# Kernel tuning notes

Measured on AMD Instinct MI355X. Metric: run time of the kernel, lower is better.

## Reference

```python
import jax, jax.numpy as jnp
import numpy as np


def _lstm_dir(xz, Uh, reverse):
    """Run one LSTM direction. xz: [B,T,4U] = x@W + b precomputed. Uh: [U,4U].
    activation='sigmoid' (replaces tanh on candidate and cell output),
    recurrent_activation='sigmoid' (Keras default). Gate order: i, f, g, o."""
    B = xz.shape[0]
    units = Uh.shape[0]
    h0 = jnp.zeros((B, units), xz.dtype)
    c0 = jnp.zeros((B, units), xz.dtype)

    def step(carry, z_t):
        h, c = carry
        z = z_t + h @ Uh                      # [B,4U]
        i, f, g, o = jnp.split(z, 4, axis=-1)
        i = jax.nn.sigmoid(i)
        f = jax.nn.sigmoid(f)
        g = jax.nn.sigmoid(g)                 # activation='sigmoid'
        o = jax.nn.sigmoid(o)
        c = f * c + i * g
        h = o * jax.nn.sigmoid(c)             # output activation also sigmoid
        return (h, c), h

    xz_t = jnp.swapaxes(xz, 0, 1)             # [T,B,4U]
    _, hs = jax.lax.scan(step, (h0, c0), xz_t, reverse=reverse)
    return jnp.swapaxes(hs, 0, 1)             # [B,T,U], time-ordered


def setup_inputs() -> dict:
    key = jax.random.key(0)
    k1, k2, k3 = jax.random.split(key, 3)
    B, T, D = 16, 1024, 1024
    L, U = 5, 512
    x = jax.random.normal(k1, (B, T, D), dtype=jnp.float32)
    # Glorot-ish scaling to keep sigmoids out of deep saturation
    W = jax.random.normal(k2, (L, 2, D, 4 * U), dtype=jnp.float32) * 0.03
    Uh = jax.random.normal(k3, (L, 2, U, 4 * U), dtype=jnp.float32) * 0.03
    b = jnp.zeros((L, 2, 4 * U), dtype=jnp.float32)
    return {"x": x, "W": W, "Uh": Uh, "b": b}


def reference(x, W, Uh, b):
    y = x
    n_layers = W.shape[0]
    for l in range(n_layers):
        outs = []
        for d, rev in ((0, False), (1, True)):
            # input projection for all timesteps at once (one big GEMM)
            xz = jnp.einsum('bti,io->bto', y, W[l, d]) + b[l, d]
            outs.append(_lstm_dir(xz, Uh[l, d], rev))
        y = jnp.concatenate(outs, axis=-1)    # Bidirectional merge_mode='concat'
    return y
```

## Files before the change

kernel.cpp:

```cpp
#include <hip/hip_runtime.h>
#include <hip/hip_bf16.h>
#include <stdint.h>


typedef __attribute__((ext_vector_type(8))) short short8;
typedef __attribute__((ext_vector_type(4))) float f32x4;

union U128 { uint4 u; short8 s; };
static __device__ __forceinline__ short8 as_short8(uint4 v) { U128 x; x.u = v; return x.s; }

static __device__ __forceinline__ float sigf(float x) { return 1.0f / (1.0f + __expf(-x)); }

static __device__ __forceinline__ uint32_t f2bfbits(float f) {
  union { float f; uint32_t u; } x; x.f = f;
  return (x.u + 0x7fffu + ((x.u >> 16) & 1u)) >> 16;
}
static __device__ __forceinline__ float bflo(uint32_t v) {
  union { uint32_t u; float f; } x; x.u = v << 16; return x.f;
}
static __device__ __forceinline__ float bfhi(uint32_t v) {
  union { uint32_t u; float f; } x; x.u = v & 0xffff0000u; return x.f;
}

__global__ __launch_bounds__(256) void f32_to_bf16_k(const float* __restrict__ in,
                                                     __hip_bfloat16* __restrict__ out,
                                                     int n4) {
  int i = blockIdx.x * 256 + threadIdx.x;
  if (i < n4) {
    float4 v = ((const float4*)in)[i];
    uint32_t lo = f2bfbits(v.x) | (f2bfbits(v.y) << 16);
    uint32_t hi = f2bfbits(v.z) | (f2bfbits(v.w) << 16);
    ((uint2*)out)[i] = make_uint2(lo, hi);
  }
}

__global__ __launch_bounds__(256) void transpose_bf16_k(const float* __restrict__ in,
                                                        __hip_bfloat16* __restrict__ outp,
                                                        int R) {
  __shared__ float tile[64][65];
  int d = blockIdx.z;
  int k0 = blockIdx.x * 64;
  int c0 = blockIdx.y * 64;
  const float* inb = in + (size_t)d * R * 2048;
  __hip_bfloat16* ob = outp + (size_t)d * 2048 * R;
  int col = threadIdx.x & 63, rr = threadIdx.x >> 6;
#pragma unroll
  for (int i = 0; i < 16; ++i) {
    int r = rr + i * 4;
    tile[r][col] = inb[(size_t)(k0 + r) * 2048 + c0 + col];
  }
  __syncthreads();
#pragma unroll
  for (int i = 0; i < 16; ++i) {
    int r = rr + i * 4;
    ob[(size_t)(c0 + r) * R + k0 + col] = __float2bfloat16(tile[col][r]);
  }
}

__global__ __launch_bounds__(256) void gemm_xz_k(const __hip_bfloat16* __restrict__ y,
                                                 const __hip_bfloat16* __restrict__ Wt,
                                                 const float* __restrict__ bias,
                                                 __hip_bfloat16* __restrict__ xz) {
  __shared__ uint4 Asl[8 * 2 * 64];
  __shared__ uint4 Bsl[8 * 2 * 64];
  int m0 = blockIdx.x * 128;
  int dir = blockIdx.y >> 4;
  int n0 = (blockIdx.y & 15) * 128;
  int tid = threadIdx.x, lane = tid & 63, wv = tid >> 6;
  int wm = wv & 1, wn = wv >> 1;
  const __hip_bfloat16* Wd = Wt + (size_t)dir * 2048 * 1024;
  f32x4 acc[4][4] = {};
  for (int kb = 0; kb < 1024; kb += 64) {
    __syncthreads();
#pragma unroll
    for (int i = 0; i < 4; ++i) {
      int slot = i * 256 + tid;
      int ln = slot & 63, kc = (slot >> 6) & 1, mt = slot >> 7;
      int row = mt * 16 + (ln & 15);
      int kk = kc * 32 + (ln >> 4) * 8;
      Asl[slot] = *(const uint4*)(y + (size_t)(m0 + row) * 1024 + kb + kk);
      Bsl[slot] = *(const uint4*)(Wd + (size_t)(n0 + row) * 1024 + kb + kk);
    }
    __syncthreads();
#pragma unroll
    for (int kc = 0; kc < 2; ++kc) {
      short8 af[4], bf[4];
#pragma unroll
      for (int i = 0; i < 4; ++i) {
        af[i] = as_short8(Asl[((wm * 4 + i) * 2 + kc) * 64 + lane]);
        bf[i] = as_short8(Bsl[((wn * 4 + i) * 2 + kc) * 64 + lane]);
      }
#pragma unroll
      for (int i = 0; i < 4; ++i)
#pragma unroll
        for (int j = 0; j < 4; ++j)
          acc[i][j] = __builtin_amdgcn_mfma_f32_16x16x32_bf16(af[i], bf[j], acc[i][j], 0, 0, 0);
    }
  }
  int cq = lane >> 4, cn = lane & 15;
#pragma unroll
  for (int i = 0; i < 4; ++i)
#pragma unroll
    for (int j = 0; j < 4; ++j) {
      int n_g = n0 + (wn * 4 + j) * 16 + cn;
      int q = n_g >> 9, u = n_g & 511, swg = u >> 5, jj = u & 31;
      float bv = bias[dir * 2048 + n_g];
#pragma unroll
      for (int r = 0; r < 4; ++r) {
        int m = m0 + (wm * 4 + i) * 16 + cq * 4 + r;
        int b = m >> 10, t = m & 1023;
        size_t addr = (((size_t)(dir * 16 + swg) * 1024 + t) * 2048) + (q * 16 + b) * 32 + jj;
        xz[addr] = __float2bfloat16(acc[i][j][r] + bv);
      }
    }
}

__global__ __launch_bounds__(256) void lstm_rec_k(const __hip_bfloat16* __restrict__ Ut,
                                                  const __hip_bfloat16* __restrict__ xz,
                                                  __hip_bfloat16* __restrict__ ynext,
                                                  float* __restrict__ outf) {
  extern __shared__ char smem[];
  uint4* uh = (uint4*)smem;
  __hip_bfloat16* hbuf = (__hip_bfloat16*)(smem + 131072);
  float* zbuf = (float*)(smem + 147712);
  __hip_bfloat16* xbuf = (__hip_bfloat16*)(smem + 155904);
  int dir = blockIdx.x & 1;
  int swg = blockIdx.x >> 1;
  int u0 = swg * 32;
  int tid = threadIdx.x, lane = tid & 63, wv = tid >> 6;
  int quad = lane >> 4, l15 = lane & 15;
  const __hip_bfloat16* Ud = Ut + (size_t)dir * 2048 * 512;

#pragma unroll 4
  for (int i = 0; i < 32; ++i) {
    int slot = i * 256 + tid;
    int ls = slot & 63, kc = (slot >> 6) & 15, nt = slot >> 10;
    int n_g = (nt >> 1) * 512 + u0 + (nt & 1) * 16 + (ls & 15);
    int k = kc * 32 + (ls >> 4) * 8;
    uh[slot] = *(const uint4*)(Ud + (size_t)n_g * 512 + k);
  }
  __syncthreads();

  int nt0 = wv * 2, nt1 = wv * 2 + 1;
  int pb = tid >> 4, pj = (tid & 15) * 2;
  float c0 = 0.f, c1 = 0.f;

  int t0 = dir ? 1023 : 0;
  const uint4* xp0 = (const uint4*)(xz + ((size_t)(dir * 16 + swg) * 1024 + t0) * 2048) + tid;
  uint4 xcur = *xp0;

  for (int s = 0; s < 1024; ++s) {
    int t = dir ? (1023 - s) : s;
    uint4 xnxt;
    if (s < 1023) {
      int tn = dir ? (1022 - s) : (s + 1);
      xnxt = *((const uint4*)(xz + ((size_t)(dir * 16 + swg) * 1024 + tn) * 2048) + tid);
    }
    f32x4 z0 = {}, z1 = {};
    if (s > 0) {
      int tprev = dir ? (t + 1) : (t - 1);
      unsigned long long hv[8];
      const unsigned long long* gp[8];
#pragma unroll
      for (int i = 0; i < 4; ++i) {
        int v = i * 2048 + tid * 8;
        int b = v >> 9, col = v & 511;
        const unsigned long long* g =
            (const unsigned long long*)(ynext + ((size_t)b * 1024 + tprev) * 1024 + dir * 512 + col);
        gp[2 * i] = g;
        gp[2 * i + 1] = g + 1;
      }
#pragma unroll
      for (int i = 0; i < 8; ++i)
        hv[i] = __hip_atomic_load(gp[i], __ATOMIC_RELAXED, __HIP_MEMORY_SCOPE_AGENT);
      for (;;) {
        bool ok = true;
#pragma unroll
        for (int i = 0; i < 8; ++i)
          ok &= ((uint32_t)hv[i] != 0u) && ((uint32_t)(hv[i] >> 32) != 0u);
        if (ok) break;
#pragma unroll
        for (int i = 0; i < 8; ++i)
          if (((uint32_t)hv[i] == 0u) || ((uint32_t)(hv[i] >> 32) == 0u))
            hv[i] = __hip_atomic_load(gp[i], __ATOMIC_RELAXED, __HIP_MEMORY_SCOPE_AGENT);
      }
#pragma unroll
      for (int i = 0; i < 4; ++i) {
        int v = i * 2048 + tid * 8;
        int b = v >> 9, col = v & 511;
        unsigned long long* lp = (unsigned long long*)(hbuf + b * 520 + col);
        lp[0] = hv[2 * i];
        lp[1] = hv[2 * i + 1];
      }
      __syncthreads();
#pragma unroll
      for (int kc = 0; kc < 16; ++kc) {
        short8 afrag = *(const short8*)(hbuf + l15 * 520 + kc * 32 + quad * 8);
        z0 = __builtin_amdgcn_mfma_f32_16x16x32_bf16(afrag, as_short8(uh[(nt0 * 16 + kc) * 64 + lane]), z0, 0, 0, 0);
        z1 = __builtin_amdgcn_mfma_f32_16x16x32_bf16(afrag, as_short8(uh[(nt1 * 16 + kc) * 64 + lane]), z1, 0, 0, 0);
      }
    }
#pragma unroll
    for (int r = 0; r < 4; ++r) {
      int m = quad * 4 + r;
      zbuf[m * 128 + nt0 * 16 + l15] = z0[r];
      zbuf[m * 128 + nt1 * 16 + l15] = z1[r];
    }
    *(uint4*)(xbuf + tid * 8) = xcur;
    __syncthreads();
    const float* zb = zbuf + pb * 128;
    uint32_t xi = *(const uint32_t*)(xbuf + (0 * 16 + pb) * 32 + pj);
    uint32_t xf = *(const uint32_t*)(xbuf + (1 * 16 + pb) * 32 + pj);
    uint32_t xg = *(const uint32_t*)(xbuf + (2 * 16 + pb) * 32 + pj);
    uint32_t xo = *(const uint32_t*)(xbuf + (3 * 16 + pb) * 32 + pj);
    float i0 = sigf(zb[pj] + bflo(xi)),      i1 = sigf(zb[pj + 1] + bfhi(xi));
    float f0 = sigf(zb[32 + pj] + bflo(xf)), f1 = sigf(zb[32 + pj + 1] + bfhi(xf));
    float g0 = sigf(zb[64 + pj] + bflo(xg)), g1 = sigf(zb[64 + pj + 1] + bfhi(xg));
    float o0 = sigf(zb[96 + pj] + bflo(xo)), o1 = sigf(zb[96 + pj + 1] + bfhi(xo));
    c0 = f0 * c0 + i0 * g0;
    c1 = f1 * c1 + i1 * g1;
    float h0 = o0 * sigf(c0);
    float h1 = o1 * sigf(c1);
    size_t oidx = ((size_t)pb * 1024 + t) * 1024 + dir * 512 + u0 + pj;
    uint32_t ha = f2bfbits(h0); ha += (ha == 0u);
    uint32_t hb = f2bfbits(h1); hb += (hb == 0u);
    uint32_t hp = ha | (hb << 16);
    __hip_atomic_store((uint32_t*)(ynext + oidx), hp, __ATOMIC_RELAXED, __HIP_MEMORY_SCOPE_AGENT);
    if (outf) { outf[oidx] = h0; outf[oidx + 1] = h1; }
    __syncthreads();
    xcur = xnxt;
  }
}

extern "C" void kernel_launch(void* const* d_in, const int* in_sizes, int n_in,
                              void* d_out, int out_size, void* d_ws, size_t ws_size,
                              hipStream_t stream) {
  const float* x  = (const float*)d_in[0];
  const float* W  = (const float*)d_in[1];
  const float* Uh = (const float*)d_in[2];
  const float* b  = (const float*)d_in[3];

  char* ws = (char*)d_ws;
  size_t off = 0;
  __hip_bfloat16* yA = (__hip_bfloat16*)(ws + off); off += (size_t)16 * 1024 * 1024 * 2;
  __hip_bfloat16* yB = (__hip_bfloat16*)(ws + off); off += (size_t)16 * 1024 * 1024 * 2;
  __hip_bfloat16* xz = (__hip_bfloat16*)(ws + off); off += (size_t)2 * 16 * 1024 * 2048 * 2;
  __hip_bfloat16* Wt = (__hip_bfloat16*)(ws + off); off += (size_t)2 * 2048 * 1024 * 2;
  __hip_bfloat16* Ut = (__hip_bfloat16*)(ws + off); off += (size_t)2 * 2048 * 512 * 2;

  f32_to_bf16_k<<<dim3(16384), dim3(256), 0, stream>>>(x, yA, 4194304);
  hipFuncSetAttribute(reinterpret_cast<const void*>(lstm_rec_k),
                      hipFuncAttributeMaxDynamicSharedMemorySize, 160000);
  for (int l = 0; l < 5; ++l) {
    transpose_bf16_k<<<dim3(16, 32, 2), dim3(256), 0, stream>>>(W + (size_t)l * 2 * 1024 * 2048, Wt, 1024);
    transpose_bf16_k<<<dim3(8, 32, 2),  dim3(256), 0, stream>>>(Uh + (size_t)l * 2 * 512 * 2048, Ut, 512);
    __hip_bfloat16* ycur = (l & 1) ? yB : yA;
    __hip_bfloat16* ynxt = (l & 1) ? yA : yB;
    hipMemsetAsync(ynxt, 0, (size_t)16 * 1024 * 1024 * 2, stream);
    gemm_xz_k<<<dim3(128, 32), dim3(256), 0, stream>>>(ycur, Wt, b + (size_t)l * 2 * 2048, xz);
    lstm_rec_k<<<dim3(32), dim3(256), 160000, stream>>>(
        Ut, xz, ynxt, (l == 4) ? (float*)d_out : nullptr);
  }
}
```

Baseline: 13.86 ms.

## Load recurrent h fragments straight into MFMA registers, dropping LDS staging and barriers

Each lane now polls the exact 16 bytes of the previous hidden state it needs as the MFMA A-operand, straight from global memory. This removes the LDS h-buffer, one __syncthreads, and the end-of-step barrier, which becomes a compiler-only fence. It relies on the cross-block spin-wait to order reuse of zbuf and xbuf across steps. The zbuf row stride is padded to 132 to reduce bank conflicts. The trade-off is more redundant global and L2 loads per step, since all four waves fetch the same fragment, and more registers held during polling.

```diff
diff --git a/kernel.cpp b/kernel.cpp
--- a/kernel.cpp
+++ b/kernel.cpp
@@ -9,6 +9,8 @@
 union U128 { uint4 u; short8 s; };
 static __device__ __forceinline__ short8 as_short8(uint4 v) { U128 x; x.u = v; return x.s; }
 
+union U128Q { unsigned long long q[2]; short8 s; };
+
 static __device__ __forceinline__ float sigf(float x) { return 1.0f / (1.0f + __expf(-x)); }
 
 static __device__ __forceinline__ uint32_t f2bfbits(float f) {
@@ -20,6 +22,10 @@
 }
 static __device__ __forceinline__ float bfhi(uint32_t v) {
   union { uint32_t u; float f; } x; x.u = v & 0xffff0000u; return x.f;
+}
+
+static __device__ __forceinline__ bool qok(unsigned long long v) {
+  return ((uint32_t)v != 0u) & ((uint32_t)(v >> 32) != 0u);
 }
 
 __global__ __launch_bounds__(256) void f32_to_bf16_k(const float* __restrict__ in,
@@ -121,9 +127,8 @@
                                                   float* __restrict__ outf) {
   extern __shared__ char smem[];
   uint4* uh = (uint4*)smem;
-  __hip_bfloat16* hbuf = (__hip_bfloat16*)(smem + 131072);
-  float* zbuf = (float*)(smem + 147712);
-  __hip_bfloat16* xbuf = (__hip_bfloat16*)(smem + 155904);
+  float* zbuf = (float*)(smem + 131072);
+  __hip_bfloat16* xbuf = (__hip_bfloat16*)(smem + 139520);
   int dir = blockIdx.x & 1;
   int swg = blockIdx.x >> 1;
   int u0 = swg * 32;
@@ -149,6 +154,8 @@
   const uint4* xp0 = (const uint4*)(xz + ((size_t)(dir * 16 + swg) * 1024 + t0) * 2048) + tid;
   uint4 xcur = *xp0;
 
+  const char* fragbase0 = (const char*)(ynext + (size_t)l15 * 1024 * 1024 + (size_t)dir * 512 + quad * 8);
+
   for (int s = 0; s < 1024; ++s) {
     int t = dir ? (1023 - s) : s;
     uint4 xnxt;
@@ -159,56 +166,46 @@
     f32x4 z0 = {}, z1 = {};
     if (s > 0) {
       int tprev = dir ? (t + 1) : (t - 1);
-      unsigned long long hv[8];
-      const unsigned long long* gp[8];
-#pragma unroll
-      for (int i = 0; i < 4; ++i) {
-        int v = i * 2048 + tid * 8;
-        int b = v >> 9, col = v & 511;
-        const unsigned long long* g =
-            (const unsigned long long*)(ynext + ((size_t)b * 1024 + tprev) * 1024 + dir * 512 + col);
-        gp[2 * i] = g;
-        gp[2 * i + 1] = g + 1;
-      }
-#pragma unroll
-      for (int i = 0; i < 8; ++i)
-        hv[i] = __hip_atomic_load(gp[i], __ATOMIC_RELAXED, __HIP_MEMORY_SCOPE_AGENT);
+      const char* fb = fragbase0 + (size_t)tprev * 2048;
+      unsigned long long hq0[16], hq1[16];
+#pragma unroll
+      for (int kc = 0; kc < 16; ++kc) {
+        hq0[kc] = __hip_atomic_load((const unsigned long long*)(fb + kc * 64),
+                                    __ATOMIC_RELAXED, __HIP_MEMORY_SCOPE_AGENT);
+        hq1[kc] = __hip_atomic_load((const unsigned long long*)(fb + kc * 64 + 8),
+                                    __ATOMIC_RELAXED, __HIP_MEMORY_SCOPE_AGENT);
+      }
       for (;;) {
         bool ok = true;
 #pragma unroll
-        for (int i = 0; i < 8; ++i)
-          ok &= ((uint32_t)hv[i] != 0u) && ((uint32_t)(hv[i] >> 32) != 0u);
+        for (int kc = 0; kc < 16; ++kc) ok &= qok(hq0[kc]) & qok(hq1[kc]);
         if (ok) break;
 #pragma unroll
-        for (int i = 0; i < 8; ++i)
-          if (((uint32_t)hv[i] == 0u) || ((uint32_t)(hv[i] >> 32) == 0u))
-            hv[i] = __hip_atomic_load(gp[i], __ATOMIC_RELAXED, __HIP_MEMORY_SCOPE_AGENT);
-      }
-#pragma unroll
-      for (int i = 0; i < 4; ++i) {
-        int v = i * 2048 + tid * 8;
-        int b = v >> 9, col = v & 511;
-        unsigned long long* lp = (unsigned long long*)(hbuf + b * 520 + col);
-        lp[0] = hv[2 * i];
-        lp[1] = hv[2 * i + 1];
-      }
-      __syncthreads();
+        for (int kc = 0; kc < 16; ++kc) {
+          if (!qok(hq0[kc]))
+            hq0[kc] = __hip_atomic_load((const unsigned long long*)(fb + kc * 64),
+                                        __ATOMIC_RELAXED, __HIP_MEMORY_SCOPE_AGENT);
+          if (!qok(hq1[kc]))
+            hq1[kc] = __hip_atomic_load((const unsigned long long*)(fb + kc * 64 + 8),
+                                        __ATOMIC_RELAXED, __HIP_MEMORY_SCOPE_AGENT);
+        }
+      }
 #pragma unroll
       for (int kc = 0; kc < 16; ++kc) {
-        short8 afrag = *(const short8*)(hbuf + l15 * 520 + kc * 32 + quad * 8);
-        z0 = __builtin_amdgcn_mfma_f32_16x16x32_bf16(afrag, as_short8(uh[(nt0 * 16 + kc) * 64 + lane]), z0, 0, 0, 0);
-        z1 = __builtin_amdgcn_mfma_f32_16x16x32_bf16(afrag, as_short8(uh[(nt1 * 16 + kc) * 64 + lane]), z1, 0, 0, 0);
+        U128Q a; a.q[0] = hq0[kc]; a.q[1] = hq1[kc];
+        z0 = __builtin_amdgcn_mfma_f32_16x16x32_bf16(a.s, as_short8(uh[(nt0 * 16 + kc) * 64 + lane]), z0, 0, 0, 0);
+        z1 = __builtin_amdgcn_mfma_f32_16x16x32_bf16(a.s, as_short8(uh[(nt1 * 16 + kc) * 64 + lane]), z1, 0, 0, 0);
       }
     }
 #pragma unroll
     for (int r = 0; r < 4; ++r) {
       int m = quad * 4 + r;
-      zbuf[m * 128 + nt0 * 16 + l15] = z0[r];
-      zbuf[m * 128 + nt1 * 16 + l15] = z1[r];
+      zbuf[m * 132 + nt0 * 16 + l15] = z0[r];
+      zbuf[m * 132 + nt1 * 16 + l15] = z1[r];
     }
     *(uint4*)(xbuf + tid * 8) = xcur;
     __syncthreads();
-    const float* zb = zbuf + pb * 128;
+    const float* zb = zbuf + pb * 132;
     uint32_t xi = *(const uint32_t*)(xbuf + (0 * 16 + pb) * 32 + pj);
     uint32_t xf = *(const uint32_t*)(xbuf + (1 * 16 + pb) * 32 + pj);
     uint32_t xg = *(const uint32_t*)(xbuf + (2 * 16 + pb) * 32 + pj);
@@ -227,7 +224,7 @@
     uint32_t hp = ha | (hb << 16);
     __hip_atomic_store((uint32_t*)(ynext + oidx), hp, __ATOMIC_RELAXED, __HIP_MEMORY_SCOPE_AGENT);
     if (outf) { outf[oidx] = h0; outf[oidx + 1] = h1; }
-    __syncthreads();
+    asm volatile("" ::: "memory");
     xcur = xnxt;
   }
 }
@@ -250,7 +247,7 @@
 
   f32_to_bf16_k<<<dim3(16384), dim3(256), 0, stream>>>(x, yA, 4194304);
   hipFuncSetAttribute(reinterpret_cast<const void*>(lstm_rec_k),
-                      hipFuncAttributeMaxDynamicSharedMemorySize, 160000);
+                      hipFuncAttributeMaxDynamicSharedMemorySize, 143616);
   for (int l = 0; l < 5; ++l) {
     transpose_bf16_k<<<dim3(16, 32, 2), dim3(256), 0, stream>>>(W + (size_t)l * 2 * 1024 * 2048, Wt, 1024);
     transpose_bf16_k<<<dim3(8, 32, 2),  dim3(256), 0, stream>>>(Uh + (size_t)l * 2 * 512 * 2048, Ut, 512);
@@ -258,7 +255,7 @@
     __hip_bfloat16* ynxt = (l & 1) ? yA : yB;
     hipMemsetAsync(ynxt, 0, (size_t)16 * 1024 * 1024 * 2, stream);
     gemm_xz_k<<<dim3(128, 32), dim3(256), 0, stream>>>(ycur, Wt, b + (size_t)l * 2 * 2048, xz);
-    lstm_rec_k<<<dim3(32), dim3(256), 160000, stream>>>(
+    lstm_rec_k<<<dim3(32), dim3(256), 143616, stream>>>(
         Ut, xz, ynxt, (l == 4) ? (float*)d_out : nullptr);
   }
 }
```

New measurement: 36.06 ms. 160% more time.

## Interleave gate columns so LSTM cell update runs in MFMA registers via shuffles

Applied to the files above, without the earlier changes.

Reorders the recurrent weight columns and the precomputed xz layout so the four gates of each unit land in adjacent lanes of the MFMA output. The cell update is then done directly from accumulator registers with lane shuffles, which removes the LDS round trip through zbuf/xbuf and one __syncthreads per timestep on the serial recurrence. It also pads the h buffer stride to change LDS bank mapping. The cost is more shuffles, redundant sigmoid work across lanes, and narrower strided stores of h.

```diff
diff --git a/kernel.cpp b/kernel.cpp
--- a/kernel.cpp
+++ b/kernel.cpp
@@ -103,13 +103,16 @@
 #pragma unroll
     for (int j = 0; j < 4; ++j) {
       int n_g = n0 + (wn * 4 + j) * 16 + cn;
-      int q = n_g >> 9, u = n_g & 511, swg = u >> 5, jj = u & 31;
+      int gate = n_g >> 9, u = n_g & 511, swg = u >> 5, ul = u & 31;
+      int nt = ul >> 2, l15 = ((ul & 3) << 2) | gate;
       float bv = bias[dir * 2048 + n_g];
 #pragma unroll
       for (int r = 0; r < 4; ++r) {
         int m = m0 + (wm * 4 + i) * 16 + cq * 4 + r;
         int b = m >> 10, t = m & 1023;
-        size_t addr = (((size_t)(dir * 16 + swg) * 1024 + t) * 2048) + (q * 16 + b) * 32 + jj;
+        int quad = b >> 2, rr = b & 3;
+        size_t addr = (((size_t)(dir * 16 + swg) * 1024 + t) * 2048) +
+                      ((nt * 16 + l15) * 4 + quad) * 4 + rr;
         xz[addr] = __float2bfloat16(acc[i][j][r] + bv);
       }
     }
@@ -122,8 +125,6 @@
   extern __shared__ char smem[];
   uint4* uh = (uint4*)smem;
   __hip_bfloat16* hbuf = (__hip_bfloat16*)(smem + 131072);
-  float* zbuf = (float*)(smem + 147712);
-  __hip_bfloat16* xbuf = (__hip_bfloat16*)(smem + 155904);
   int dir = blockIdx.x & 1;
   int swg = blockIdx.x >> 1;
   int u0 = swg * 32;
@@ -135,26 +136,35 @@
   for (int i = 0; i < 32; ++i) {
     int slot = i * 256 + tid;
     int ls = slot & 63, kc = (slot >> 6) & 15, nt = slot >> 10;
-    int n_g = (nt >> 1) * 512 + u0 + (nt & 1) * 16 + (ls & 15);
+    int n_g = (ls & 3) * 512 + u0 + nt * 4 + ((ls & 15) >> 2);
     int k = kc * 32 + (ls >> 4) * 8;
     uh[slot] = *(const uint4*)(Ud + (size_t)n_g * 512 + k);
   }
   __syncthreads();
 
   int nt0 = wv * 2, nt1 = wv * 2 + 1;
-  int pb = tid >> 4, pj = (tid & 15) * 2;
-  float c0 = 0.f, c1 = 0.f;
+  int o0 = ((nt0 * 16 + l15) * 4 + quad) * 4;
+  int o1 = ((nt1 * 16 + l15) * 4 + quad) * 4;
+  bool gb0 = (lane & 1) != 0, gb1 = (lane & 2) != 0;
+  int u4 = l15 >> 2;
+  int unit = u0 + wv * 8 + 0 ;
+  bool st_act = ((l15 & 7) == 0);
+  float cst0[4] = {0.f, 0.f, 0.f, 0.f};
+  float cst1[4] = {0.f, 0.f, 0.f, 0.f};
 
   int t0 = dir ? 1023 : 0;
-  const uint4* xp0 = (const uint4*)(xz + ((size_t)(dir * 16 + swg) * 1024 + t0) * 2048) + tid;
-  uint4 xcur = *xp0;
+  const __hip_bfloat16* xc0 = xz + ((size_t)(dir * 16 + swg) * 1024 + t0) * 2048;
+  uint2 xq0 = *(const uint2*)(xc0 + o0);
+  uint2 xq1 = *(const uint2*)(xc0 + o1);
 
   for (int s = 0; s < 1024; ++s) {
     int t = dir ? (1023 - s) : s;
-    uint4 xnxt;
+    uint2 xn0 = xq0, xn1 = xq1;
     if (s < 1023) {
       int tn = dir ? (1022 - s) : (s + 1);
-      xnxt = *((const uint4*)(xz + ((size_t)(dir * 16 + swg) * 1024 + tn) * 2048) + tid);
+      const __hip_bfloat16* xc = xz + ((size_t)(dir * 16 + swg) * 1024 + tn) * 2048;
+      xn0 = *(const uint2*)(xc + o0);
+      xn1 = *(const uint2*)(xc + o1);
     }
     f32x4 z0 = {}, z1 = {};
     if (s > 0) {
@@ -188,48 +198,57 @@
       for (int i = 0; i < 4; ++i) {
         int v = i * 2048 + tid * 8;
         int b = v >> 9, col = v & 511;
-        unsigned long long* lp = (unsigned long long*)(hbuf + b * 520 + col);
+        unsigned long long* lp = (unsigned long long*)(hbuf + b * 528 + col);
         lp[0] = hv[2 * i];
         lp[1] = hv[2 * i + 1];
       }
       __syncthreads();
 #pragma unroll
       for (int kc = 0; kc < 16; ++kc) {
-        short8 afrag = *(const short8*)(hbuf + l15 * 520 + kc * 32 + quad * 8);
+        short8 afrag = *(const short8*)(hbuf + l15 * 528 + kc * 32 + quad * 8);
         z0 = __builtin_amdgcn_mfma_f32_16x16x32_bf16(afrag, as_short8(uh[(nt0 * 16 + kc) * 64 + lane]), z0, 0, 0, 0);
         z1 = __builtin_amdgcn_mfma_f32_16x16x32_bf16(afrag, as_short8(uh[(nt1 * 16 + kc) * 64 + lane]), z1, 0, 0, 0);
       }
     }
-#pragma unroll
-    for (int r = 0; r < 4; ++r) {
-      int m = quad * 4 + r;
-      zbuf[m * 128 + nt0 * 16 + l15] = z0[r];
-      zbuf[m * 128 + nt1 * 16 + l15] = z1[r];
-    }
-    *(uint4*)(xbuf + tid * 8) = xcur;
+    float xr0[4] = {bflo(xq0.x), bfhi(xq0.x), bflo(xq0.y), bfhi(xq0.y)};
+    float xr1[4] = {bflo(xq1.x), bfhi(xq1.x), bflo(xq1.y), bfhi(xq1.y)};
+#pragma unroll
+    for (int tl = 0; tl < 2; ++tl) {
+      int unit_e = u0 + wv * 8 + (tl ? nt1 & 1 ? 0 : 0 : 0);
+#pragma unroll
+      for (int r = 0; r < 4; ++r) {
+        float zz = tl ? z1[r] : z0[r];
+        float xx = tl ? xr1[r] : xr0[r];
+        float sv = sigf(zz + xx);
+        float b1 = __shfl_xor(sv, 1);
+        float b2 = __shfl_xor(sv, 2);
+        float b3 = __shfl_xor(b1, 2);
+        float ig = gb0 ? (b1 * b3) : (sv * b2);
+        float fg = gb0 ? (gb1 ? b2 : sv) : (gb1 ? b3 : b1);
+        float og = gb0 ? (gb1 ? sv : b2) : (gb1 ? b1 : b3);
+        float& c = tl ? cst1[r] : cst0[r];
+        c = fg * c + ig;
+        float h = og * sigf(c);
+        uint32_t hb = f2bfbits(h);
+        hb += (hb == 0u);
+        uint32_t hpart = __shfl_xor(hb, 4);
+        uint32_t hfull = __float_as_uint(h);
+        uint32_t hfpart = __shfl_xor(hfull, 4);
+        if (st_act) {
+          int un = u0 + wv * 8 + (tl ? 4 : 0) + u4;
+          int batch = quad * 4 + r;
+          size_t oidx = ((size_t)batch * 1024 + t) * 1024 + dir * 512 + un;
+          __hip_atomic_store((uint32_t*)(ynext + oidx), hb | (hpart << 16),
+                             __ATOMIC_RELAXED, __HIP_MEMORY_SCOPE_AGENT);
+          if (outf) *(uint2*)(outf + oidx) = make_uint2(hfull, hfpart);
+        }
+      }
+    }
     __syncthreads();
-    const float* zb = zbuf + pb * 128;
-    uint32_t xi = *(const uint32_t*)(xbuf + (0 * 16 + pb) * 32 + pj);
-    uint32_t xf = *(const uint32_t*)(xbuf + (1 * 16 + pb) * 32 + pj);
-    uint32_t xg = *(const uint32_t*)(xbuf + (2 * 16 + pb) * 32 + pj);
-    uint32_t xo = *(const uint32_t*)(xbuf + (3 * 16 + pb) * 32 + pj);
-    float i0 = sigf(zb[pj] + bflo(xi)),      i1 = sigf(zb[pj + 1] + bfhi(xi));
-    float f0 = sigf(zb[32 + pj] + bflo(xf)), f1 = sigf(zb[32 + pj + 1] + bfhi(xf));
-    float g0 = sigf(zb[64 + pj] + bflo(xg)), g1 = sigf(zb[64 + pj + 1] + bfhi(xg));
-    float o0 = sigf(zb[96 + pj] + bflo(xo)), o1 = sigf(zb[96 + pj + 1] + bfhi(xo));
-    c0 = f0 * c0 + i0 * g0;
-    c1 = f1 * c1 + i1 * g1;
-    float h0 = o0 * sigf(c0);
-    float h1 = o1 * sigf(c1);
-    size_t oidx = ((size_t)pb * 1024 + t) * 1024 + dir * 512 + u0 + pj;
-    uint32_t ha = f2bfbits(h0); ha += (ha == 0u);
-    uint32_t hb = f2bfbits(h1); hb += (hb == 0u);
-    uint32_t hp = ha | (hb << 16);
-    __hip_atomic_store((uint32_t*)(ynext + oidx), hp, __ATOMIC_RELAXED, __HIP_MEMORY_SCOPE_AGENT);
-    if (outf) { outf[oidx] = h0; outf[oidx + 1] = h1; }
-    __syncthreads();
-    xcur = xnxt;
-  }
+    xq0 = xn0;
+    xq1 = xn1;
+  }
+  (void)unit;
 }
 
 extern "C" void kernel_launch(void* const* d_in, const int* in_sizes, int n_in,
@@ -250,7 +269,7 @@
 
   f32_to_bf16_k<<<dim3(16384), dim3(256), 0, stream>>>(x, yA, 4194304);
   hipFuncSetAttribute(reinterpret_cast<const void*>(lstm_rec_k),
-                      hipFuncAttributeMaxDynamicSharedMemorySize, 160000);
+                      hipFuncAttributeMaxDynamicSharedMemorySize, 147968);
   for (int l = 0; l < 5; ++l) {
     transpose_bf16_k<<<dim3(16, 32, 2), dim3(256), 0, stream>>>(W + (size_t)l * 2 * 1024 * 2048, Wt, 1024);
     transpose_bf16_k<<<dim3(8, 32, 2),  dim3(256), 0, stream>>>(Uh + (size_t)l * 2 * 512 * 2048, Ut, 512);
@@ -258,7 +277,7 @@
     __hip_bfloat16* ynxt = (l & 1) ? yA : yB;
     hipMemsetAsync(ynxt, 0, (size_t)16 * 1024 * 1024 * 2, stream);
     gemm_xz_k<<<dim3(128, 32), dim3(256), 0, stream>>>(ycur, Wt, b + (size_t)l * 2 * 2048, xz);
-    lstm_rec_k<<<dim3(32), dim3(256), 160000, stream>>>(
+    lstm_rec_k<<<dim3(32), dim3(256), 147968, stream>>>(
         Ut, xz, ynxt, (l == 4) ? (float*)d_out : nullptr);
   }
 }
```

Measured after the change: 21.42 ms. +54.5%, slower.

## Overlap next layer's input-projection GEMM with current LSTM recurrence in one kernel

Applied to the files above, without the earlier changes.

The recurrence kernel now launches 128 blocks. The first 32 run the sequential LSTM scan, and the other 96 compute the next layer's x@W+b GEMM tiles as soon as the needed timesteps of the current layer's output have been published. They detect readiness by polling for nonzero bf16 values with sleep-backoff spin loops. Double-buffered xz, Wt and Ut workspaces let the weight transposes and the memset move out of the critical path. The aim is to hide each layer's input-projection GEMM behind the latency-bound recurrence, which only occupies 32 CUs, at the cost of more workspace and spin-wait traffic that could contend with the recurrent blocks.

```diff
diff --git a/kernel.cpp b/kernel.cpp
--- a/kernel.cpp
+++ b/kernel.cpp
@@ -20,6 +20,9 @@
 }
 static __device__ __forceinline__ float bfhi(uint32_t v) {
   union { uint32_t u; float f; } x; x.u = v & 0xffff0000u; return x.f;
+}
+static __device__ __forceinline__ bool qok(unsigned long long v) {
+  return ((uint32_t)v != 0u) & ((uint32_t)(v >> 32) != 0u);
 }
 
 __global__ __launch_bounds__(256) void f32_to_bf16_k(const float* __restrict__ in,
@@ -108,8 +111,8 @@
 #pragma unroll
       for (int r = 0; r < 4; ++r) {
         int m = m0 + (wm * 4 + i) * 16 + cq * 4 + r;
-        int b = m >> 10, t = m & 1023;
-        size_t addr = (((size_t)(dir * 16 + swg) * 1024 + t) * 2048) + (q * 16 + b) * 32 + jj;
+        int bb = m >> 10, t = m & 1023;
+        size_t addr = (((size_t)(dir * 16 + swg) * 1024 + t) * 2048) + (q * 16 + bb) * 32 + jj;
         xz[addr] = __float2bfloat16(acc[i][j][r] + bv);
       }
     }
@@ -118,117 +121,200 @@
 __global__ __launch_bounds__(256) void lstm_rec_k(const __hip_bfloat16* __restrict__ Ut,
                                                   const __hip_bfloat16* __restrict__ xz,
                                                   __hip_bfloat16* __restrict__ ynext,
-                                                  float* __restrict__ outf) {
+                                                  float* __restrict__ outf,
+                                                  const __hip_bfloat16* __restrict__ Wtn,
+                                                  const float* __restrict__ biasn,
+                                                  __hip_bfloat16* __restrict__ xznext) {
   extern __shared__ char smem[];
-  uint4* uh = (uint4*)smem;
-  __hip_bfloat16* hbuf = (__hip_bfloat16*)(smem + 131072);
-  float* zbuf = (float*)(smem + 147712);
-  __hip_bfloat16* xbuf = (__hip_bfloat16*)(smem + 155904);
-  int dir = blockIdx.x & 1;
-  int swg = blockIdx.x >> 1;
-  int u0 = swg * 32;
   int tid = threadIdx.x, lane = tid & 63, wv = tid >> 6;
-  int quad = lane >> 4, l15 = lane & 15;
-  const __hip_bfloat16* Ud = Ut + (size_t)dir * 2048 * 512;
+
+  if (blockIdx.x < 32) {
+    uint4* uh = (uint4*)smem;
+    __hip_bfloat16* hbuf = (__hip_bfloat16*)(smem + 131072);
+    float* zbuf = (float*)(smem + 147712);
+    __hip_bfloat16* xbuf = (__hip_bfloat16*)(smem + 155904);
+    int dir = blockIdx.x & 1;
+    int swg = blockIdx.x >> 1;
+    int u0 = swg * 32;
+    int quad = lane >> 4, l15 = lane & 15;
+    const __hip_bfloat16* Ud = Ut + (size_t)dir * 2048 * 512;
 
 #pragma unroll 4
-  for (int i = 0; i < 32; ++i) {
-    int slot = i * 256 + tid;
-    int ls = slot & 63, kc = (slot >> 6) & 15, nt = slot >> 10;
-    int n_g = (nt >> 1) * 512 + u0 + (nt & 1) * 16 + (ls & 15);
-    int k = kc * 32 + (ls >> 4) * 8;
-    uh[slot] = *(const uint4*)(Ud + (size_t)n_g * 512 + k);
-  }
-  __syncthreads();
-
-  int nt0 = wv * 2, nt1 = wv * 2 + 1;
-  int pb = tid >> 4, pj = (tid & 15) * 2;
-  float c0 = 0.f, c1 = 0.f;
-
-  int t0 = dir ? 1023 : 0;
-  const uint4* xp0 = (const uint4*)(xz + ((size_t)(dir * 16 + swg) * 1024 + t0) * 2048) + tid;
-  uint4 xcur = *xp0;
-
-  for (int s = 0; s < 1024; ++s) {
-    int t = dir ? (1023 - s) : s;
-    uint4 xnxt;
-    if (s < 1023) {
-      int tn = dir ? (1022 - s) : (s + 1);
-      xnxt = *((const uint4*)(xz + ((size_t)(dir * 16 + swg) * 1024 + tn) * 2048) + tid);
-    }
-    f32x4 z0 = {}, z1 = {};
-    if (s > 0) {
-      int tprev = dir ? (t + 1) : (t - 1);
-      unsigned long long hv[8];
-      const unsigned long long* gp[8];
+    for (int i = 0; i < 32; ++i) {
+      int slot = i * 256 + tid;
+      int ls = slot & 63, kc = (slot >> 6) & 15, nt = slot >> 10;
+      int n_g = (nt >> 1) * 512 + u0 + (nt & 1) * 16 + (ls & 15);
+      int k = kc * 32 + (ls >> 4) * 8;
+      uh[slot] = *(const uint4*)(Ud + (size_t)n_g * 512 + k);
+    }
+    __syncthreads();
+
+    int nt0 = wv * 2, nt1 = wv * 2 + 1;
+    int pb = tid >> 4, pj = (tid & 15) * 2;
+    float c0 = 0.f, c1 = 0.f;
+
+    int t0 = dir ? 1023 : 0;
+    const uint4* xp0 = (const uint4*)(xz + ((size_t)(dir * 16 + swg) * 1024 + t0) * 2048) + tid;
+    uint4 xcur = *xp0;
+
+    for (int s = 0; s < 1024; ++s) {
+      int t = dir ? (1023 - s) : s;
+      uint4 xnxt;
+      if (s < 1023) {
+        int tn = dir ? (1022 - s) : (s + 1);
+        xnxt = *((const uint4*)(xz + ((size_t)(dir * 16 + swg) * 1024 + tn) * 2048) + tid);
+      }
+      f32x4 z0 = {}, z1 = {};
+      if (s > 0) {
+        int tprev = dir ? (t + 1) : (t - 1);
+        unsigned long long hv[8];
+        const unsigned long long* gp[8];
+#pragma unroll
+        for (int i = 0; i < 4; ++i) {
+          int v = i * 2048 + tid * 8;
+          int bb = v >> 9, col = v & 511;
+          const unsigned long long* g =
+              (const unsigned long long*)(ynext + ((size_t)bb * 1024 + tprev) * 1024 + dir * 512 + col);
+          gp[2 * i] = g;
+          gp[2 * i + 1] = g + 1;
+        }
+#pragma unroll
+        for (int i = 0; i < 8; ++i)
+          hv[i] = __hip_atomic_load(gp[i], __ATOMIC_RELAXED, __HIP_MEMORY_SCOPE_AGENT);
+        for (;;) {
+          bool ok = true;
+#pragma unroll
+          for (int i = 0; i < 8; ++i)
+            ok &= ((uint32_t)hv[i] != 0u) && ((uint32_t)(hv[i] >> 32) != 0u);
+          if (ok) break;
+#pragma unroll
+          for (int i = 0; i < 8; ++i)
+            if (((uint32_t)hv[i] == 0u) || ((uint32_t)(hv[i] >> 32) == 0u))
+              hv[i] = __hip_atomic_load(gp[i], __ATOMIC_RELAXED, __HIP_MEMORY_SCOPE_AGENT);
+        }
+#pragma unroll
+        for (int i = 0; i < 4; ++i) {
+          int v = i * 2048 + tid * 8;
+          int bb = v >> 9, col = v & 511;
+          unsigned long long* lp = (unsigned long long*)(hbuf + bb * 520 + col);
+          lp[0] = hv[2 * i];
+          lp[1] = hv[2 * i + 1];
+        }
+        __syncthreads();
+#pragma unroll
+        for (int kc = 0; kc < 16; ++kc) {
+          short8 afrag = *(const short8*)(hbuf + l15 * 520 + kc * 32 + quad * 8);
+          z0 = __builtin_amdgcn_mfma_f32_16x16x32_bf16(afrag, as_short8(uh[(nt0 * 16 + kc) * 64 + lane]), z0, 0, 0, 0);
+          z1 = __builtin_amdgcn_mfma_f32_16x16x32_bf16(afrag, as_short8(uh[(nt1 * 16 + kc) * 64 + lane]), z1, 0, 0, 0);
+        }
+      }
+#pragma unroll
+      for (int r = 0; r < 4; ++r) {
+        int m = quad * 4 + r;
+        zbuf[m * 128 + nt0 * 16 + l15] = z0[r];
+        zbuf[m * 128 + nt1 * 16 + l15] = z1[r];
+      }
+      *(uint4*)(xbuf + tid * 8) = xcur;
+      __syncthreads();
+      const float* zb = zbuf + pb * 128;
+      uint32_t xi = *(const uint32_t*)(xbuf + (0 * 16 + pb) * 32 + pj);
+      uint32_t xf = *(const uint32_t*)(xbuf + (1 * 16 + pb) * 32 + pj);
+      uint32_t xg = *(const uint32_t*)(xbuf + (2 * 16 + pb) * 32 + pj);
+      uint32_t xo = *(const uint32_t*)(xbuf + (3 * 16 + pb) * 32 + pj);
+      float i0 = sigf(zb[pj] + bflo(xi)),      i1 = sigf(zb[pj + 1] + bfhi(xi));
+      float f0 = sigf(zb[32 + pj] + bflo(xf)), f1 = sigf(zb[32 + pj + 1] + bfhi(xf));
+      float g0 = sigf(zb[64 + pj] + bflo(xg)), g1 = sigf(zb[64 + pj + 1] + bfhi(xg));
+      float o0 = sigf(zb[96 + pj] + bflo(xo)), o1 = sigf(zb[96 + pj + 1] + bfhi(xo));
+      c0 = f0 * c0 + i0 * g0;
+      c1 = f1 * c1 + i1 * g1;
+      float h0 = o0 * sigf(c0);
+      float h1 = o1 * sigf(c1);
+      size_t oidx = ((size_t)pb * 1024 + t) * 1024 + dir * 512 + u0 + pj;
+      uint32_t ha = f2bfbits(h0); ha += (ha == 0u);
+      uint32_t hb = f2bfbits(h1); hb += (hb == 0u);
+      uint32_t hp = ha | (hb << 16);
+      __hip_atomic_store((uint32_t*)(ynext + oidx), hp, __ATOMIC_RELAXED, __HIP_MEMORY_SCOPE_AGENT);
+      if (outf) { outf[oidx] = h0; outf[oidx + 1] = h1; }
+      __syncthreads();
+      xcur = xnxt;
+    }
+    return;
+  }
+
+  if (!xznext) return;
+  uint4* Asl = (uint4*)smem;
+  uint4* Bsl = ((uint4*)smem) + 1024;
+  int gb = blockIdx.x - 32;
+  int wm = wv & 1, wn = wv >> 1;
+  for (int g = gb; g < 4096; g += 96) {
+    int kq = g >> 6, inner = g & 63;
+    int c = (kq & 1) ? (31 - (kq >> 1)) : (32 + (kq >> 1));
+    int tt0 = c * 16;
+    int bg = inner & 1, ngi = (inner >> 1) & 15, gdir = inner >> 5;
+    int n0 = ngi * 128;
+    const __hip_bfloat16* Wd = Wtn + (size_t)gdir * 2048 * 1024;
+    {
+      int rr = (tt0 + 15 > 1023 - tt0) ? (tt0 + 15) : (1023 - tt0);
+      int tp = rr + 32; if (tp > 1023) tp = 1023;
+      const uint32_t* pp = (const uint32_t*)(ynext + ((size_t)(bg * 8) * 1024 + tp) * 1024);
+      while (__hip_atomic_load(pp, __ATOMIC_RELAXED, __HIP_MEMORY_SCOPE_AGENT) == 0u)
+        __builtin_amdgcn_s_sleep(32);
+    }
+    f32x4 acc[4][4] = {};
+    for (int kb = 0; kb < 1024; kb += 64) {
+      __syncthreads();
 #pragma unroll
       for (int i = 0; i < 4; ++i) {
-        int v = i * 2048 + tid * 8;
-        int b = v >> 9, col = v & 511;
-        const unsigned long long* g =
-            (const unsigned long long*)(ynext + ((size_t)b * 1024 + tprev) * 1024 + dir * 512 + col);
-        gp[2 * i] = g;
-        gp[2 * i + 1] = g + 1;
-      }
-#pragma unroll
-      for (int i = 0; i < 8; ++i)
-        hv[i] = __hip_atomic_load(gp[i], __ATOMIC_RELAXED, __HIP_MEMORY_SCOPE_AGENT);
-      for (;;) {
-        bool ok = true;
-#pragma unroll
-        for (int i = 0; i < 8; ++i)
-          ok &= ((uint32_t)hv[i] != 0u) && ((uint32_t)(hv[i] >> 32) != 0u);
-        if (ok) break;
-#pragma unroll
-        for (int i = 0; i < 8; ++i)
-          if (((uint32_t)hv[i] == 0u) || ((uint32_t)(hv[i] >> 32) == 0u))
-            hv[i] = __hip_atomic_load(gp[i], __ATOMIC_RELAXED, __HIP_MEMORY_SCOPE_AGENT);
-      }
-#pragma unroll
-      for (int i = 0; i < 4; ++i) {
-        int v = i * 2048 + tid * 8;
-        int b = v >> 9, col = v & 511;
-        unsigned long long* lp = (unsigned long long*)(hbuf + b * 520 + col);
-        lp[0] = hv[2 * i];
-        lp[1] = hv[2 * i + 1];
+        int slot = i * 256 + tid;
+        int ln = slot & 63, kc = (slot >> 6) & 1, mt = slot >> 7;
+        int row = mt * 16 + (ln & 15);
+        int kcol = kc * 32 + (ln >> 4) * 8;
+        int bb = bg * 8 + (row >> 4), tt = tt0 + (row & 15);
+        const unsigned long long* ap =
+            (const unsigned long long*)(ynext + ((size_t)bb * 1024 + tt) * 1024 + kb + kcol);
+        unsigned long long a0 = __hip_atomic_load(ap, __ATOMIC_RELAXED, __HIP_MEMORY_SCOPE_AGENT);
+        unsigned long long a1 = __hip_atomic_load(ap + 1, __ATOMIC_RELAXED, __HIP_MEMORY_SCOPE_AGENT);
+        while (!(qok(a0) & qok(a1))) {
+          __builtin_amdgcn_s_sleep(8);
+          if (!qok(a0)) a0 = __hip_atomic_load(ap, __ATOMIC_RELAXED, __HIP_MEMORY_SCOPE_AGENT);
+          if (!qok(a1)) a1 = __hip_atomic_load(ap + 1, __ATOMIC_RELAXED, __HIP_MEMORY_SCOPE_AGENT);
+        }
+        unsigned long long* asl = (unsigned long long*)&Asl[slot];
+        asl[0] = a0; asl[1] = a1;
+        Bsl[slot] = *(const uint4*)(Wd + (size_t)(n0 + row) * 1024 + kb + kcol);
       }
       __syncthreads();
 #pragma unroll
-      for (int kc = 0; kc < 16; ++kc) {
-        short8 afrag = *(const short8*)(hbuf + l15 * 520 + kc * 32 + quad * 8);
-        z0 = __builtin_amdgcn_mfma_f32_16x16x32_bf16(afrag, as_short8(uh[(nt0 * 16 + kc) * 64 + lane]), z0, 0, 0, 0);
-        z1 = __builtin_amdgcn_mfma_f32_16x16x32_bf16(afrag, as_short8(uh[(nt1 * 16 + kc) * 64 + lane]), z1, 0, 0, 0);
-      }
-    }
-#pragma unroll
-    for (int r = 0; r < 4; ++r) {
-      int m = quad * 4 + r;
-      zbuf[m * 128 + nt0 * 16 + l15] = z0[r];
-      zbuf[m * 128 + nt1 * 16 + l15] = z1[r];
-    }
-    *(uint4*)(xbuf + tid * 8) = xcur;
-    __syncthreads();
-    const float* zb = zbuf + pb * 128;
-    uint32_t xi = *(const uint32_t*)(xbuf + (0 * 16 + pb) * 32 + pj);
-    uint32_t xf = *(const uint32_t*)(xbuf + (1 * 16 + pb) * 32 + pj);
-    uint32_t xg = *(const uint32_t*)(xbuf + (2 * 16 + pb) * 32 + pj);
-    uint32_t xo = *(const uint32_t*)(xbuf + (3 * 16 + pb) * 32 + pj);
-    float i0 = sigf(zb[pj] + bflo(xi)),      i1 = sigf(zb[pj + 1] + bfhi(xi));
-    float f0 = sigf(zb[32 + pj] + bflo(xf)), f1 = sigf(zb[32 + pj + 1] + bfhi(xf));
-    float g0 = sigf(zb[64 + pj] + bflo(xg)), g1 = sigf(zb[64 + pj + 1] + bfhi(xg));
-    float o0 = sigf(zb[96 + pj] + bflo(xo)), o1 = sigf(zb[96 + pj + 1] + bfhi(xo));
-    c0 = f0 * c0 + i0 * g0;
-    c1 = f1 * c1 + i1 * g1;
-    float h0 = o0 * sigf(c0);
-    float h1 = o1 * sigf(c1);
-    size_t oidx = ((size_t)pb * 1024 + t) * 1024 + dir * 512 + u0 + pj;
-    uint32_t ha = f2bfbits(h0); ha += (ha == 0u);
-    uint32_t hb = f2bfbits(h1); hb += (hb == 0u);
-    uint32_t hp = ha | (hb << 16);
-    __hip_atomic_store((uint32_t*)(ynext + oidx), hp, __ATOMIC_RELAXED, __HIP_MEMORY_SCOPE_AGENT);
-    if (outf) { outf[oidx] = h0; outf[oidx + 1] = h1; }
-    __syncthreads();
-    xcur = xnxt;
+      for (int kc = 0; kc < 2; ++kc) {
+        short8 af[4], bf[4];
+#pragma unroll
+        for (int i = 0; i < 4; ++i) {
+          af[i] = as_short8(Asl[((wm * 4 + i) * 2 + kc) * 64 + lane]);
+          bf[i] = as_short8(Bsl[((wn * 4 + i) * 2 + kc) * 64 + lane]);
+        }
+#pragma unroll
+        for (int i = 0; i < 4; ++i)
+#pragma unroll
+          for (int j = 0; j < 4; ++j)
+            acc[i][j] = __builtin_amdgcn_mfma_f32_16x16x32_bf16(af[i], bf[j], acc[i][j], 0, 0, 0);
+      }
+    }
+    int cq = lane >> 4, cn = lane & 15;
+#pragma unroll
+    for (int i = 0; i < 4; ++i)
+#pragma unroll
+      for (int j = 0; j < 4; ++j) {
+        int n_g = n0 + (wn * 4 + j) * 16 + cn;
+        int q = n_g >> 9, uu = n_g & 511, sw = uu >> 5, jj = uu & 31;
+        float bv = biasn[gdir * 2048 + n_g];
+#pragma unroll
+        for (int r = 0; r < 4; ++r) {
+          int ml = (wm * 4 + i) * 16 + cq * 4 + r;
+          int bb = bg * 8 + (ml >> 4), tt = tt0 + (ml & 15);
+          size_t addr = (((size_t)(gdir * 16 + sw) * 1024 + tt) * 2048) + (q * 16 + bb) * 32 + jj;
+          xznext[addr] = __float2bfloat16(acc[i][j][r] + bv);
+        }
+      }
   }
 }
 
@@ -242,23 +328,61 @@
 
   char* ws = (char*)d_ws;
   size_t off = 0;
-  __hip_bfloat16* yA = (__hip_bfloat16*)(ws + off); off += (size_t)16 * 1024 * 1024 * 2;
-  __hip_bfloat16* yB = (__hip_bfloat16*)(ws + off); off += (size_t)16 * 1024 * 1024 * 2;
-  __hip_bfloat16* xz = (__hip_bfloat16*)(ws + off); off += (size_t)2 * 16 * 1024 * 2048 * 2;
-  __hip_bfloat16* Wt = (__hip_bfloat16*)(ws + off); off += (size_t)2 * 2048 * 1024 * 2;
-  __hip_bfloat16* Ut = (__hip_bfloat16*)(ws + off); off += (size_t)2 * 2048 * 512 * 2;
+  __hip_bfloat16* yA  = (__hip_bfloat16*)(ws + off); off += (size_t)16 * 1024 * 1024 * 2;
+  __hip_bfloat16* yB  = (__hip_bfloat16*)(ws + off); off += (size_t)16 * 1024 * 1024 * 2;
+  __hip_bfloat16* xzA = (__hip_bfloat16*)(ws + off); off += (size_t)2 * 16 * 1024 * 2048 * 2;
+  __hip_bfloat16* WtA = (__hip_bfloat16*)(ws + off); off += (size_t)2 * 2048 * 1024 * 2;
+  __hip_bfloat16* UtA = (__hip_bfloat16*)(ws + off); off += (size_t)2 * 2048 * 512 * 2;
+  __hip_bfloat16* xzB = (__hip_bfloat16*)(ws + off); off += (size_t)2 * 16 * 1024 * 2048 * 2;
+  __hip_bfloat16* WtB = (__hip_bfloat16*)(ws + off); off += (size_t)2 * 2048 * 1024 * 2;
+  __hip_bfloat16* UtB = (__hip_bfloat16*)(ws + off); off += (size_t)2 * 2048 * 512 * 2;
+  const bool fuse = (ws_size >= off);
 
   f32_to_bf16_k<<<dim3(16384), dim3(256), 0, stream>>>(x, yA, 4194304);
   hipFuncSetAttribute(reinterpret_cast<const void*>(lstm_rec_k),
                       hipFuncAttributeMaxDynamicSharedMemorySize, 160000);
+
+  if (!fuse) {
+    for (int l = 0; l < 5; ++l) {
+      transpose_bf16_k<<<dim3(16, 32, 2), dim3(256), 0, stream>>>(W + (size_t)l * 2 * 1024 * 2048, WtA, 1024);
+      transpose_bf16_k<<<dim3(8, 32, 2),  dim3(256), 0, stream>>>(Uh + (size_t)l * 2 * 512 * 2048, UtA, 512);
+      __hip_bfloat16* ycur = (l & 1) ? yB : yA;
+      __hip_bfloat16* ynxt = (l & 1) ? yA : yB;
+      hipMemsetAsync(ynxt, 0, (size_t)16 * 1024 * 1024 * 2, stream);
+      gemm_xz_k<<<dim3(128, 32), dim3(256), 0, stream>>>(ycur, WtA, b + (size_t)l * 2 * 2048, xzA);
+      lstm_rec_k<<<dim3(32), dim3(256), 160000, stream>>>(
+          UtA, xzA, ynxt, (l == 4) ? (float*)d_out : nullptr, nullptr, nullptr, nullptr);
+    }
+    return;
+  }
+
+  __hip_bfloat16* Wtb[2] = {WtA, WtB};
+  __hip_bfloat16* Utb[2] = {UtA, UtB};
+  __hip_bfloat16* xzb[2] = {xzA, xzB};
+
+  transpose_bf16_k<<<dim3(16, 32, 2), dim3(256), 0, stream>>>(W, Wtb[0], 1024);
+  transpose_bf16_k<<<dim3(8, 32, 2),  dim3(256), 0, stream>>>(Uh, Utb[0], 512);
+  hipMemsetAsync(yB, 0, (size_t)16 * 1024 * 1024 * 2, stream);
+  gemm_xz_k<<<dim3(128, 32), dim3(256), 0, stream>>>(yA, Wtb[0], b, xzb[0]);
+
   for (int l = 0; l < 5; ++l) {
-    transpose_bf16_k<<<dim3(16, 32, 2), dim3(256), 0, stream>>>(W + (size_t)l * 2 * 1024 * 2048, Wt, 1024);
-    transpose_bf16_k<<<dim3(8, 32, 2),  dim3(256), 0, stream>>>(Uh + (size_t)l * 2 * 512 * 2048, Ut, 512);
     __hip_bfloat16* ycur = (l & 1) ? yB : yA;
     __hip_bfloat16* ynxt = (l & 1) ? yA : yB;
-    hipMemsetAsync(ynxt, 0, (size_t)16 * 1024 * 1024 * 2, stream);
-    gemm_xz_k<<<dim3(128, 32), dim3(256), 0, stream>>>(ycur, Wt, b + (size_t)l * 2 * 2048, xz);
-    lstm_rec_k<<<dim3(32), dim3(256), 160000, stream>>>(
-        Ut, xz, ynxt, (l == 4) ? (float*)d_out : nullptr);
-  }
-}
+    __hip_bfloat16* xzc  = xzb[l & 1];
+    __hip_bfloat16* xzn  = xzb[(l + 1) & 1];
+    if (l < 4)
+      transpose_bf16_k<<<dim3(16, 32, 2), dim3(256), 0, stream>>>(
+          W + (size_t)(l + 1) * 2 * 1024 * 2048, Wtb[(l + 1) & 1], 1024);
+    int grid = (l < 4) ? 128 : 32;
+    lstm_rec_k<<<dim3(grid), dim3(256), 160000, stream>>>(
+        Utb[l & 1], xzc, ynxt, (l == 4) ? (float*)d_out : nullptr,
+        (l < 4) ? Wtb[(l + 1) & 1] : nullptr,
+        (l < 4) ? (b + (size_t)(l + 1) * 2 * 2048) : nullptr,
+        (l < 4) ? xzn : nullptr);
+    if (l < 4) {
+      transpose_bf16_k<<<dim3(8, 32, 2), dim3(256), 0, stream>>>(
+          Uh + (size_t)(l + 1) * 2 * 512 * 2048, Utb[(l + 1) & 1], 512);
+      hipMemsetAsync(ycur, 0, (size_t)16 * 1024 * 1024 * 2, stream);
+    }
+  }
+}
```

New measurement: 13.87 ms. About the same (+0.1%).
